# Kernel tuning notes

Measured on AMD Instinct MI355X. Metric: run time of the kernel, lower is better.

## Reference

```python
import jax, jax.numpy as jnp
import numpy as np

EPS = 1e-06


def setup_inputs() -> dict:
    key = jax.random.key(0)
    B, T, M = 64, 8000, 80
    x = jax.random.uniform(key, (B, T, M), dtype=jnp.float32)
    # learned params are stored in log-space, per-mel, matching the torch module
    log_s = jnp.full((M,), np.log(0.0001), dtype=jnp.float32)
    log_alpha = jnp.full((M,), np.log(0.98), dtype=jnp.float32)
    log_delta = jnp.full((M,), np.log(2.0), dtype=jnp.float32)
    log_r = jnp.full((M,), np.log(0.2), dtype=jnp.float32)
    return {"x": x, "log_s": log_s, "log_alpha": log_alpha,
            "log_delta": log_delta, "log_r": log_r}


def reference(x, log_s, log_alpha, log_delta, log_r):
    # PCEN: leaky-integrator EMA over time + power-law compression.
    s = jnp.exp(log_s)          # [M]
    alpha = jnp.exp(log_alpha)  # [M]
    delta = jnp.exp(log_delta)  # [M]
    r = jnp.exp(log_r)          # [M]
    delta_r = delta ** r

    B, T, M = x.shape
    xt = jnp.swapaxes(x, 0, 1)  # [T, B, M] so scan streams over time

    def step(m_prev, frame):  # m_prev, frame: [B, M]
        m_cur = (1.0 - s) * m_prev + s * frame
        out = (frame / (m_cur + EPS) ** alpha + delta) ** r - delta_r
        return m_cur, out

    m0 = jnp.zeros((B, M), dtype=x.dtype)
    _, out_t = jax.lax.scan(step, m0, xt)  # [T, B, M]
    return jnp.swapaxes(out_t, 0, 1)       # [B, T, M]
```

## Files before the change

kernel.cpp:

```cpp
#include <hip/hip_runtime.h>
#include <math.h>

#define PCEN_EPS 1e-6f

__global__ __launch_bounds__(256) void pcen_chunk_scan_v4(
    const float4* __restrict__ x,
    const float* __restrict__ log_s,
    float4* __restrict__ contrib,
    int B, int T, int G, int C, int L)
{
    int tid = blockIdx.x * blockDim.x + threadIdx.x;
    int total = B * C * G;
    if (tid >= total) return;
    int g = tid % G;
    int c = (tid / G) % C;
    int b = tid / (G * C);

    const float4 lsv = ((const float4*)log_s)[g];
    const float sx = expf(lsv.x), sy = expf(lsv.y), sz = expf(lsv.z), sw = expf(lsv.w);
    const float ox = 1.0f - sx, oy = 1.0f - sy, oz = 1.0f - sz, ow = 1.0f - sw;

    const int start = c * L;
    int len = T - start;
    if (len > L) len = L;
    if (len < 0) len = 0;

    int p = (b * T + start) * G + g;
    float mx = 0.f, my = 0.f, mz = 0.f, mw = 0.f;
#pragma unroll 8
    for (int i = 0; i < len; ++i) {
        float4 xv = x[p];
        mx = fmaf(ox, mx, sx * xv.x);
        my = fmaf(oy, my, sy * xv.y);
        mz = fmaf(oz, mz, sz * xv.z);
        mw = fmaf(ow, mw, sw * xv.w);
        p += G;
    }
    float4 o; o.x = mx; o.y = my; o.z = mz; o.w = mw;
    contrib[tid] = o;
}

__global__ __launch_bounds__(256) void pcen_output_v4(
    const float4* __restrict__ x,
    const float* __restrict__ log_s,
    const float* __restrict__ log_alpha,
    const float* __restrict__ log_delta,
    const float* __restrict__ log_r,
    const float4* __restrict__ contrib,
    float4* __restrict__ out,
    int B, int T, int G, int C, int L)
{
    int tid = blockIdx.x * blockDim.x + threadIdx.x;
    int total = B * C * G;
    if (tid >= total) return;
    int g = tid % G;
    int c = (tid / G) % C;
    int b = tid / (G * C);

    const float4 lsv = ((const float4*)log_s)[g];
    const float sx = expf(lsv.x), sy = expf(lsv.y), sz = expf(lsv.z), sw = expf(lsv.w);
    const float ox = 1.0f - sx, oy = 1.0f - sy, oz = 1.0f - sz, ow = 1.0f - sw;

    const float dLx = powf(ox, (float)L);
    const float dLy = powf(oy, (float)L);
    const float dLz = powf(oz, (float)L);
    const float dLw = powf(ow, (float)L);

    float mx = 0.f, my = 0.f, mz = 0.f, mw = 0.f;
    {
        float wx = 1.f, wy = 1.f, wz = 1.f, ww = 1.f;
        const int base = b * C * G + g;
#pragma unroll 4
        for (int j = c - 1; j >= 0; --j) {
            float4 v = contrib[base + j * G];
            mx = fmaf(wx, v.x, mx);
            my = fmaf(wy, v.y, my);
            mz = fmaf(wz, v.z, mz);
            mw = fmaf(ww, v.w, mw);
            wx *= dLx; wy *= dLy; wz *= dLz; ww *= dLw;
        }
    }

    const float4 lav = ((const float4*)log_alpha)[g];
    const float4 ldv = ((const float4*)log_delta)[g];
    const float4 lrv = ((const float4*)log_r)[g];
    const float ax = expf(lav.x), ay = expf(lav.y), az = expf(lav.z), aw = expf(lav.w);
    const float dx = expf(ldv.x), dy = expf(ldv.y), dz = expf(ldv.z), dw = expf(ldv.w);
    const float rx = expf(lrv.x), ry = expf(lrv.y), rz = expf(lrv.z), rw = expf(lrv.w);
    const float drx = powf(dx, rx), dry = powf(dy, ry);
    const float drz = powf(dz, rz), drw = powf(dw, rw);

    const int start = c * L;
    int len = T - start;
    if (len > L) len = L;
    if (len < 0) len = 0;

    int p = (b * T + start) * G + g;
#pragma unroll 4
    for (int i = 0; i < len; ++i) {
        float4 xv = x[p];
        mx = fmaf(ox, mx, sx * xv.x);
        my = fmaf(oy, my, sy * xv.y);
        mz = fmaf(oz, mz, sz * xv.z);
        mw = fmaf(ow, mw, sw * xv.w);

        float4 o;
        float px = __expf(-ax * __logf(mx + PCEN_EPS));
        float py = __expf(-ay * __logf(my + PCEN_EPS));
        float pz = __expf(-az * __logf(mz + PCEN_EPS));
        float pw = __expf(-aw * __logf(mw + PCEN_EPS));
        float yx = fmaf(xv.x, px, dx);
        float yy = fmaf(xv.y, py, dy);
        float yz = fmaf(xv.z, pz, dz);
        float yw = fmaf(xv.w, pw, dw);
        o.x = __expf(rx * __logf(yx)) - drx;
        o.y = __expf(ry * __logf(yy)) - dry;
        o.z = __expf(rz * __logf(yz)) - drz;
        o.w = __expf(rw * __logf(yw)) - drw;

        out[p] = o;
        p += G;
    }
}

__global__ void pcen_chunk_scan(const float* __restrict__ x,
                                const float* __restrict__ log_s,
                                float* __restrict__ contrib,
                                int B, int T, int M, int C, int L) {
    int tid = blockIdx.x * blockDim.x + threadIdx.x;
    int total = B * C * M;
    if (tid >= total) return;
    int mi = tid % M;
    int c  = (tid / M) % C;
    int b  = tid / (M * C);

    float s   = expf(log_s[mi]);
    float oms = 1.0f - s;

    int start = c * L;
    int len = T - start;
    if (len > L) len = L;
    if (len < 0) len = 0;

    int base = (b * T + start) * M + mi;
    float m = 0.0f;
#pragma unroll 4
    for (int i = 0; i < len; ++i) {
        m = fmaf(oms, m, s * x[base]);
        base += M;
    }
    contrib[tid] = m;
}

__global__ void pcen_chunk_prefix(const float* __restrict__ contrib,
                                  const float* __restrict__ log_s,
                                  float* __restrict__ m_start,
                                  int B, int T, int M, int C, int L) {
    int tid = blockIdx.x * blockDim.x + threadIdx.x;
    if (tid >= B * M) return;
    int mi = tid % M;
    int b  = tid / M;

    float s   = expf(log_s[mi]);
    float oms = 1.0f - s;
    float dL_full = powf(oms, (float)L);

    int base = b * C * M + mi;
    float m = 0.0f;
    for (int c = 0; c < C; ++c) {
        m_start[base + c * M] = m;
        int start = c * L;
        int len = T - start;
        if (len > L) len = L;
        if (len < 0) len = 0;
        float dL = (len == L) ? dL_full : powf(oms, (float)len);
        m = fmaf(dL, m, contrib[base + c * M]);
    }
}

__global__ void pcen_output(const float* __restrict__ x,
                            const float* __restrict__ log_s,
                            const float* __restrict__ log_alpha,
                            const float* __restrict__ log_delta,
                            const float* __restrict__ log_r,
                            const float* __restrict__ m_start,
                            float* __restrict__ out,
                            int B, int T, int M, int C, int L) {
    int tid = blockIdx.x * blockDim.x + threadIdx.x;
    int total = B * C * M;
    if (tid >= total) return;
    int mi = tid % M;
    int c  = (tid / M) % C;
    int b  = tid / (M * C);

    float s     = expf(log_s[mi]);
    float alpha = expf(log_alpha[mi]);
    float delta = expf(log_delta[mi]);
    float r     = expf(log_r[mi]);
    float delta_r = powf(delta, r);
    float oms   = 1.0f - s;

    int start = c * L;
    int len = T - start;
    if (len > L) len = L;
    if (len < 0) len = 0;

    float m = m_start[tid];
    int base = (b * T + start) * M + mi;
#pragma unroll 4
    for (int i = 0; i < len; ++i) {
        float xv = x[base];
        m = fmaf(oms, m, s * xv);
        float p = __expf(-alpha * __logf(m + PCEN_EPS));
        float y = fmaf(xv, p, delta);
        out[base] = __expf(r * __logf(y)) - delta_r;
        base += M;
    }
}

extern "C" void kernel_launch(void* const* d_in, const int* in_sizes, int n_in,
                              void* d_out, int out_size, void* d_ws, size_t ws_size,
                              hipStream_t stream) {
    const float* x         = (const float*)d_in[0];
    const float* log_s     = (const float*)d_in[1];
    const float* log_alpha = (const float*)d_in[2];
    const float* log_delta = (const float*)d_in[3];
    const float* log_r     = (const float*)d_in[4];
    float* out = (float*)d_out;

    const int M = in_sizes[1];
    const int B = 64;
    const int T = in_sizes[0] / (B * M);

    if ((M & 3) == 0) {
        const int G = M / 4;
        int C = 160;
        while (C > 1 && (size_t)((long long)B * C * G * 16ll) > ws_size) --C;
        int L = (T + C - 1) / C;
        C = (T + L - 1) / L;

        float4* contrib = (float4*)d_ws;

        const int total = B * C * G;
        const int blocks = (total + 255) / 256;
        pcen_chunk_scan_v4<<<blocks, 256, 0, stream>>>(
            (const float4*)x, log_s, contrib, B, T, G, C, L);
        pcen_output_v4<<<blocks, 256, 0, stream>>>(
            (const float4*)x, log_s, log_alpha, log_delta, log_r,
            contrib, (float4*)out, B, T, G, C, L);
    } else {
        int C = 50;
        while (C > 1 && (size_t)(2ll * B * C * M * 4) > ws_size) C--;
        const int L = (T + C - 1) / C;

        float* contrib = (float*)d_ws;
        float* mstart  = contrib + (size_t)B * C * M;

        const int threads = 256;
        int total1 = B * C * M;
        int total2 = B * M;
        pcen_chunk_scan<<<(total1 + threads - 1) / threads, threads, 0, stream>>>(
            x, log_s, contrib, B, T, M, C, L);
        pcen_chunk_prefix<<<(total2 + threads - 1) / threads, threads, 0, stream>>>(
            contrib, log_s, mstart, B, T, M, C, L);
        pcen_output<<<(total1 + threads - 1) / threads, threads, 0, stream>>>(
            x, log_s, log_alpha, log_delta, log_r, mstart, out, B, T, M, C, L);
    }
}
```

Measured before the change: 357.4 us.

## Software-pipeline x loads with a 4-deep register prefetch in the PCEN scan kernels

Both the chunk-scan and output kernels now preload four timesteps of x into registers and rotate through them. Each load is issued several steps before its value is consumed, so memory latency can overlap the serial EMA recurrence. The chunk length is now fixed at 48 instead of being derived from a target chunk count, and the scan kernel skips the last chunk because its contribution is never read. The risks are higher register pressure from the prefetch buffers and a longer cross-chunk prefix loop, since there are more chunks.

```diff
diff --git a/kernel.cpp b/kernel.cpp
--- a/kernel.cpp
+++ b/kernel.cpp
@@ -2,6 +2,32 @@
 #include <math.h>
 
 #define PCEN_EPS 1e-6f
+
+#define EMA_STEP(BUF)                      \
+    mx = fmaf(ox, mx, sx * (BUF).x);       \
+    my = fmaf(oy, my, sy * (BUF).y);       \
+    mz = fmaf(oz, mz, sz * (BUF).z);       \
+    mw = fmaf(ow, mw, sw * (BUF).w);
+
+#define PCEN_STEP(BUF)                                        \
+    {                                                         \
+        EMA_STEP(BUF)                                         \
+        float4 o_;                                            \
+        float px_ = __expf(-ax * __logf(mx + PCEN_EPS));      \
+        float py_ = __expf(-ay * __logf(my + PCEN_EPS));      \
+        float pz_ = __expf(-az * __logf(mz + PCEN_EPS));      \
+        float pw_ = __expf(-aw * __logf(mw + PCEN_EPS));      \
+        float yx_ = fmaf((BUF).x, px_, dx);                   \
+        float yy_ = fmaf((BUF).y, py_, dy);                   \
+        float yz_ = fmaf((BUF).z, pz_, dz);                   \
+        float yw_ = fmaf((BUF).w, pw_, dw);                   \
+        o_.x = __expf(rx * __logf(yx_)) - drx;                \
+        o_.y = __expf(ry * __logf(yy_)) - dry;                \
+        o_.z = __expf(rz * __logf(yz_)) - drz;                \
+        o_.w = __expf(rw * __logf(yw_)) - drw;                \
+        out[ps] = o_;                                         \
+        ps += G;                                              \
+    }
 
 __global__ __launch_bounds__(256) void pcen_chunk_scan_v4(
     const float4* __restrict__ x,
@@ -15,6 +41,7 @@
     int g = tid % G;
     int c = (tid / G) % C;
     int b = tid / (G * C);
+    if (c == C - 1) return;
 
     const float4 lsv = ((const float4*)log_s)[g];
     const float sx = expf(lsv.x), sy = expf(lsv.y), sz = expf(lsv.z), sw = expf(lsv.w);
@@ -23,19 +50,38 @@
     const int start = c * L;
     int len = T - start;
     if (len > L) len = L;
-    if (len < 0) len = 0;
 
     int p = (b * T + start) * G + g;
     float mx = 0.f, my = 0.f, mz = 0.f, mw = 0.f;
-#pragma unroll 8
-    for (int i = 0; i < len; ++i) {
-        float4 xv = x[p];
-        mx = fmaf(ox, mx, sx * xv.x);
-        my = fmaf(oy, my, sy * xv.y);
-        mz = fmaf(oz, mz, sz * xv.z);
-        mw = fmaf(ow, mw, sw * xv.w);
-        p += G;
-    }
+
+    if (len >= 4) {
+        float4 b0 = x[p];
+        float4 b1 = x[p + G];
+        float4 b2 = x[p + 2 * G];
+        float4 b3 = x[p + 3 * G];
+        int pl = p + 4 * G;
+        const int n_main = len - 4;
+        int i = 0;
+        for (; i + 4 <= n_main; i += 4) {
+            EMA_STEP(b0) b0 = x[pl]; pl += G;
+            EMA_STEP(b1) b1 = x[pl]; pl += G;
+            EMA_STEP(b2) b2 = x[pl]; pl += G;
+            EMA_STEP(b3) b3 = x[pl]; pl += G;
+        }
+        const int r = n_main - i;
+        if (r > 0) { EMA_STEP(b0) b0 = x[pl]; pl += G; }
+        if (r > 1) { EMA_STEP(b1) b1 = x[pl]; pl += G; }
+        if (r > 2) { EMA_STEP(b2) b2 = x[pl]; pl += G; }
+        switch (r) {
+            case 0: EMA_STEP(b0) EMA_STEP(b1) EMA_STEP(b2) EMA_STEP(b3) break;
+            case 1: EMA_STEP(b1) EMA_STEP(b2) EMA_STEP(b3) EMA_STEP(b0) break;
+            case 2: EMA_STEP(b2) EMA_STEP(b3) EMA_STEP(b0) EMA_STEP(b1) break;
+            default: EMA_STEP(b3) EMA_STEP(b0) EMA_STEP(b1) EMA_STEP(b2) break;
+        }
+    } else {
+        for (int i = 0; i < len; ++i) { float4 xv = x[p]; EMA_STEP(xv) p += G; }
+    }
+
     float4 o; o.x = mx; o.y = my; o.z = mz; o.w = mw;
     contrib[tid] = o;
 }
@@ -69,10 +115,10 @@
     float mx = 0.f, my = 0.f, mz = 0.f, mw = 0.f;
     {
         float wx = 1.f, wy = 1.f, wz = 1.f, ww = 1.f;
-        const int base = b * C * G + g;
+        const int cb = b * C * G + g;
 #pragma unroll 4
         for (int j = c - 1; j >= 0; --j) {
-            float4 v = contrib[base + j * G];
+            float4 v = contrib[cb + j * G];
             mx = fmaf(wx, v.x, mx);
             my = fmaf(wy, v.y, my);
             mz = fmaf(wz, v.z, mz);
@@ -96,30 +142,34 @@
     if (len < 0) len = 0;
 
     int p = (b * T + start) * G + g;
-#pragma unroll 4
-    for (int i = 0; i < len; ++i) {
-        float4 xv = x[p];
-        mx = fmaf(ox, mx, sx * xv.x);
-        my = fmaf(oy, my, sy * xv.y);
-        mz = fmaf(oz, mz, sz * xv.z);
-        mw = fmaf(ow, mw, sw * xv.w);
-
-        float4 o;
-        float px = __expf(-ax * __logf(mx + PCEN_EPS));
-        float py = __expf(-ay * __logf(my + PCEN_EPS));
-        float pz = __expf(-az * __logf(mz + PCEN_EPS));
-        float pw = __expf(-aw * __logf(mw + PCEN_EPS));
-        float yx = fmaf(xv.x, px, dx);
-        float yy = fmaf(xv.y, py, dy);
-        float yz = fmaf(xv.z, pz, dz);
-        float yw = fmaf(xv.w, pw, dw);
-        o.x = __expf(rx * __logf(yx)) - drx;
-        o.y = __expf(ry * __logf(yy)) - dry;
-        o.z = __expf(rz * __logf(yz)) - drz;
-        o.w = __expf(rw * __logf(yw)) - drw;
-
-        out[p] = o;
-        p += G;
+    int ps = p;
+
+    if (len >= 4) {
+        float4 b0 = x[p];
+        float4 b1 = x[p + G];
+        float4 b2 = x[p + 2 * G];
+        float4 b3 = x[p + 3 * G];
+        int pl = p + 4 * G;
+        const int n_main = len - 4;
+        int i = 0;
+        for (; i + 4 <= n_main; i += 4) {
+            PCEN_STEP(b0) b0 = x[pl]; pl += G;
+            PCEN_STEP(b1) b1 = x[pl]; pl += G;
+            PCEN_STEP(b2) b2 = x[pl]; pl += G;
+            PCEN_STEP(b3) b3 = x[pl]; pl += G;
+        }
+        const int r = n_main - i;
+        if (r > 0) { PCEN_STEP(b0) b0 = x[pl]; pl += G; }
+        if (r > 1) { PCEN_STEP(b1) b1 = x[pl]; pl += G; }
+        if (r > 2) { PCEN_STEP(b2) b2 = x[pl]; pl += G; }
+        switch (r) {
+            case 0: PCEN_STEP(b0) PCEN_STEP(b1) PCEN_STEP(b2) PCEN_STEP(b3) break;
+            case 1: PCEN_STEP(b1) PCEN_STEP(b2) PCEN_STEP(b3) PCEN_STEP(b0) break;
+            case 2: PCEN_STEP(b2) PCEN_STEP(b3) PCEN_STEP(b0) PCEN_STEP(b1) break;
+            default: PCEN_STEP(b3) PCEN_STEP(b0) PCEN_STEP(b1) PCEN_STEP(b2) break;
+        }
+    } else {
+        for (int i = 0; i < len; ++i) { float4 xv = x[p]; PCEN_STEP(xv) p += G; }
     }
 }
 
@@ -234,15 +284,17 @@
 
     if ((M & 3) == 0) {
         const int G = M / 4;
-        int C = 160;
-        while (C > 1 && (size_t)((long long)B * C * G * 16ll) > ws_size) --C;
-        int L = (T + C - 1) / C;
-        C = (T + L - 1) / L;
+        int L = 48;
+        int C = (T + L - 1) / L;
+        while ((size_t)((long long)B * C * G * 16ll) > ws_size && L < T) {
+            L += 4;
+            C = (T + L - 1) / L;
+        }
 
         float4* contrib = (float4*)d_ws;
-
         const int total = B * C * G;
         const int blocks = (total + 255) / 256;
+
         pcen_chunk_scan_v4<<<blocks, 256, 0, stream>>>(
             (const float4*)x, log_s, contrib, B, T, G, C, L);
         pcen_output_v4<<<blocks, 256, 0, stream>>>(
```

Result: no change. 359.3 us (+0.5%).

## Add Kogge-Stone chunk prefix kernel and shrink chunk length for more parallelism

Applied to the files above, without the earlier changes.

Replaces the per-thread serial O(C) reduction over earlier chunk contributions in the output kernel with a separate shared-memory Kogge-Stone scan kernel that computes each chunk's starting state once. With the cross-chunk cost now logarithmic, chunk length drops to about 20 (C up to 512 chunks), raising thread count and shortening the serial time loop. The chunk-scan kernel also skips the last chunk, whose contribution is never used. It adds a third launch and workspace for the start states.

```diff
diff --git a/kernel.cpp b/kernel.cpp
--- a/kernel.cpp
+++ b/kernel.cpp
@@ -15,6 +15,7 @@
     int g = tid % G;
     int c = (tid / G) % C;
     int b = tid / (G * C);
+    if (c == C - 1) return;
 
     const float4 lsv = ((const float4*)log_s)[g];
     const float sx = expf(lsv.x), sy = expf(lsv.y), sz = expf(lsv.z), sw = expf(lsv.w);
@@ -23,11 +24,10 @@
     const int start = c * L;
     int len = T - start;
     if (len > L) len = L;
-    if (len < 0) len = 0;
 
     int p = (b * T + start) * G + g;
     float mx = 0.f, my = 0.f, mz = 0.f, mw = 0.f;
-#pragma unroll 8
+#pragma unroll 4
     for (int i = 0; i < len; ++i) {
         float4 xv = x[p];
         mx = fmaf(ox, mx, sx * xv.x);
@@ -40,13 +40,59 @@
     contrib[tid] = o;
 }
 
+__global__ __launch_bounds__(512) void pcen_chunk_prefix_ks(
+    const float4* __restrict__ contrib,
+    const float* __restrict__ log_s,
+    float4* __restrict__ m_start,
+    int B, int G, int C, int L)
+{
+    __shared__ float4 A[512];
+    const int bg = blockIdx.x;
+    const int g = bg % G;
+    const int b = bg / G;
+    const int c = (int)threadIdx.x;
+
+    const float4 lsv = ((const float4*)log_s)[g];
+    float wx = powf(1.0f - expf(lsv.x), (float)L);
+    float wy = powf(1.0f - expf(lsv.y), (float)L);
+    float wz = powf(1.0f - expf(lsv.z), (float)L);
+    float ww = powf(1.0f - expf(lsv.w), (float)L);
+
+    float4 v = make_float4(0.f, 0.f, 0.f, 0.f);
+    if (c < C - 1) v = contrib[(b * C + c) * G + g];
+    if (c < C) A[c] = v;
+    __syncthreads();
+
+    for (int o = 1; o < C; o <<= 1) {
+        float4 left;
+        const bool act = (c >= o) && (c < C);
+        if (act) left = A[c - o];
+        __syncthreads();
+        if (act) {
+            float4 cur = A[c];
+            cur.x = fmaf(wx, left.x, cur.x);
+            cur.y = fmaf(wy, left.y, cur.y);
+            cur.z = fmaf(wz, left.z, cur.z);
+            cur.w = fmaf(ww, left.w, cur.w);
+            A[c] = cur;
+        }
+        __syncthreads();
+        wx *= wx; wy *= wy; wz *= wz; ww *= ww;
+    }
+
+    if (c < C) {
+        float4 ms = (c == 0) ? make_float4(0.f, 0.f, 0.f, 0.f) : A[c - 1];
+        m_start[(b * C + c) * G + g] = ms;
+    }
+}
+
 __global__ __launch_bounds__(256) void pcen_output_v4(
     const float4* __restrict__ x,
     const float* __restrict__ log_s,
     const float* __restrict__ log_alpha,
     const float* __restrict__ log_delta,
     const float* __restrict__ log_r,
-    const float4* __restrict__ contrib,
+    const float4* __restrict__ m_start,
     float4* __restrict__ out,
     int B, int T, int G, int C, int L)
 {
@@ -60,26 +106,6 @@
     const float4 lsv = ((const float4*)log_s)[g];
     const float sx = expf(lsv.x), sy = expf(lsv.y), sz = expf(lsv.z), sw = expf(lsv.w);
     const float ox = 1.0f - sx, oy = 1.0f - sy, oz = 1.0f - sz, ow = 1.0f - sw;
-
-    const float dLx = powf(ox, (float)L);
-    const float dLy = powf(oy, (float)L);
-    const float dLz = powf(oz, (float)L);
-    const float dLw = powf(ow, (float)L);
-
-    float mx = 0.f, my = 0.f, mz = 0.f, mw = 0.f;
-    {
-        float wx = 1.f, wy = 1.f, wz = 1.f, ww = 1.f;
-        const int base = b * C * G + g;
-#pragma unroll 4
-        for (int j = c - 1; j >= 0; --j) {
-            float4 v = contrib[base + j * G];
-            mx = fmaf(wx, v.x, mx);
-            my = fmaf(wy, v.y, my);
-            mz = fmaf(wz, v.z, mz);
-            mw = fmaf(ww, v.w, mw);
-            wx *= dLx; wy *= dLy; wz *= dLz; ww *= dLw;
-        }
-    }
 
     const float4 lav = ((const float4*)log_alpha)[g];
     const float4 ldv = ((const float4*)log_delta)[g];
@@ -94,6 +120,9 @@
     int len = T - start;
     if (len > L) len = L;
     if (len < 0) len = 0;
+
+    float4 m0 = m_start[tid];
+    float mx = m0.x, my = m0.y, mz = m0.z, mw = m0.w;
 
     int p = (b * T + start) * G + g;
 #pragma unroll 4
@@ -234,20 +263,27 @@
 
     if ((M & 3) == 0) {
         const int G = M / 4;
-        int C = 160;
-        while (C > 1 && (size_t)((long long)B * C * G * 16ll) > ws_size) --C;
-        int L = (T + C - 1) / C;
-        C = (T + L - 1) / L;
+        int L = 20;
+        int C = (T + L - 1) / L;
+        while (C > 512 ||
+               (size_t)(2ll * B * C * G * 16ll) > ws_size) {
+            L += 4;
+            C = (T + L - 1) / L;
+        }
 
         float4* contrib = (float4*)d_ws;
+        float4* mstart  = contrib + (size_t)B * C * G;
 
         const int total = B * C * G;
         const int blocks = (total + 255) / 256;
+
         pcen_chunk_scan_v4<<<blocks, 256, 0, stream>>>(
             (const float4*)x, log_s, contrib, B, T, G, C, L);
+        pcen_chunk_prefix_ks<<<B * G, 512, 0, stream>>>(
+            contrib, log_s, mstart, B, G, C, L);
         pcen_output_v4<<<blocks, 256, 0, stream>>>(
             (const float4*)x, log_s, log_alpha, log_delta, log_r,
-            contrib, (float4*)out, B, T, G, C, L);
+            mstart, (float4*)out, B, T, G, C, L);
     } else {
         int C = 50;
         while (C > 1 && (size_t)(2ll * B * C * M * 4) > ws_size) C--;
```

Result: faster. 345.4 us (-3.4%).
